# Kernel optimization log

Hardware: AMD Instinct MI355X
Metric: run time of the kernel (lower is better)

Reference implementation:

```python
import jax, jax.numpy as jnp
import numpy as np

N, K, D = 50000, 32, 128


def setup_inputs() -> dict:
    key = jax.random.key(0)
    k1, k2, k3, k4 = jax.random.split(key, 4)
    v_fea = jax.random.normal(k1, (N, D), dtype=jnp.float32)
    t_emb = jax.random.normal(k2, (N, D), dtype=jnp.float32)
    ef = jax.random.randint(k3, (N, K), 0, N, dtype=jnp.int64)
    # nn.Linear(2D, 2D, bias=False) weight, scaled like torch default init
    W = jax.random.normal(k4, (2 * D, 2 * D), dtype=jnp.float32) * (1.0 / np.sqrt(2 * D))
    return {"v_fea": v_fea, "t_emb": t_emb, "ef": ef, "W": W}


def reference(v_fea, t_emb, ef, W):
    # v: gathered neighbor features [N, K, D]
    v = v_fea[ef]
    # q: [N, 2D]; torch Linear applies x @ W.T
    q = jnp.concatenate([v_fea, t_emb], axis=-1)
    wq = q @ W.T                                   # [N, 2D]
    # k: [N, K, 2D]
    k = jnp.concatenate([v, t_emb[ef]], axis=-1)
    # per-edge score: bmm(k, wq[..., None]) -> [N, K]
    r = jnp.einsum("nkd,nd->nk", k, wq)
    r = jax.nn.softmax(r, axis=1)                  # softmax over neighbors
    # weighted sum over neighbors -> [N, D]
    ef_fea = jnp.einsum("nk,nkd->nd", r, v)
    return ef_fea
```

## Files before the change

kernel.cpp:

```cpp
#include <hip/hip_runtime.h>
#include <hip/hip_bf16.h>

#define D     128
#define TWO_D 256
#define KNB   32

typedef __attribute__((ext_vector_type(8))) short    s8;
typedef __attribute__((ext_vector_type(8))) _Float16 h8;
typedef __attribute__((ext_vector_type(2))) _Float16 h2v;
typedef __attribute__((ext_vector_type(4))) float    f4;

__device__ inline unsigned short f2h(float f) {
    return __builtin_bit_cast(unsigned short, (_Float16)f);
}
__device__ inline float h2f(unsigned short u) {
    return (float)__builtin_bit_cast(_Float16, u);
}

union v16u { s8 s; h2v h[4]; };

__device__ inline float dot8(s8 x, s8 w, float acc) {
#if __has_builtin(__builtin_amdgcn_fdot2)
    v16u ux, uw; ux.s = x; uw.s = w;
#pragma unroll
    for (int j = 0; j < 4; ++j)
        acc = __builtin_amdgcn_fdot2(ux.h[j], uw.h[j], acc, false);
#else
#pragma unroll
    for (int j = 0; j < 8; ++j)
        acc = fmaf(h2f((unsigned short)x[j]), h2f((unsigned short)w[j]), acc);
#endif
    return acc;
}

__global__ __launch_bounds__(256) void cast_kernel(
    const float* __restrict__ a, const float* __restrict__ b,
    unsigned short* __restrict__ oa, unsigned short* __restrict__ ob, int n4)
{
    int i = blockIdx.x * 256 + threadIdx.x;
    if (i >= n4) return;
    float4 x = ((const float4*)a)[i];
    float4 y = ((const float4*)b)[i];
    ushort4 px = make_ushort4(f2h(x.x), f2h(x.y), f2h(x.z), f2h(x.w));
    ushort4 py = make_ushort4(f2h(y.x), f2h(y.y), f2h(y.z), f2h(y.w));
    ((ushort4*)oa)[i] = px;
    ((ushort4*)ob)[i] = py;
}

#define BM 128
#define BN 128
#define BK 32
#define LDT 56

__global__ __launch_bounds__(256) void gemm_wq_mfma(
    const unsigned short* __restrict__ vh, const unsigned short* __restrict__ th,
    const float* __restrict__ W, unsigned short* __restrict__ wq_h, int M)
{
    __shared__ unsigned short As[BM][LDT];
    __shared__ unsigned short Bs[BN][LDT];

    const int tid  = threadIdx.x;
    const int w    = tid >> 6;
    const int lane = tid & 63;
    const int quad = lane >> 4;
    const int l16  = lane & 15;
    const int row0 = blockIdx.x * BM;
    const int i0   = blockIdx.y * BN;

    f4 acc[2][8] = {};

    const int srow = tid >> 1;
    const int seg  = tid & 1;
    int ga = row0 + srow; if (ga >= M) ga = M - 1;

    for (int kt = 0; kt < TWO_D; kt += BK) {
        const unsigned short* srcA = (kt < D) ? vh : th;
        const int kb = kt & (D - 1);
        const unsigned short* pa = srcA + (size_t)ga * D + kb + seg * 16;
        s8 a0 = *(const s8*)(pa);
        s8 a1 = *(const s8*)(pa + 8);
        const float* pb = W + (size_t)(i0 + srow) * TWO_D + kt + seg * 16;
        float4 b0 = *(const float4*)(pb);
        float4 b1 = *(const float4*)(pb + 4);
        float4 b2 = *(const float4*)(pb + 8);
        float4 b3 = *(const float4*)(pb + 12);

        __syncthreads();
        *(s8*)&As[srow][seg * 16]     = a0;
        *(s8*)&As[srow][seg * 16 + 8] = a1;
        {
            s8 q0, q1;
            q0[0]=(short)f2h(b0.x); q0[1]=(short)f2h(b0.y); q0[2]=(short)f2h(b0.z); q0[3]=(short)f2h(b0.w);
            q0[4]=(short)f2h(b1.x); q0[5]=(short)f2h(b1.y); q0[6]=(short)f2h(b1.z); q0[7]=(short)f2h(b1.w);
            q1[0]=(short)f2h(b2.x); q1[1]=(short)f2h(b2.y); q1[2]=(short)f2h(b2.z); q1[3]=(short)f2h(b2.w);
            q1[4]=(short)f2h(b3.x); q1[5]=(short)f2h(b3.y); q1[6]=(short)f2h(b3.z); q1[7]=(short)f2h(b3.w);
            *(s8*)&Bs[srow][seg * 16]     = q0;
            *(s8*)&Bs[srow][seg * 16 + 8] = q1;
        }
        __syncthreads();

        s8 af0 = *(const s8*)&As[w * 32 + l16][quad * 8];
        s8 af1 = *(const s8*)&As[w * 32 + 16 + l16][quad * 8];
#pragma unroll
        for (int nt = 0; nt < 8; ++nt) {
            s8 bf = *(const s8*)&Bs[nt * 16 + l16][quad * 8];
            acc[0][nt] = __builtin_amdgcn_mfma_f32_16x16x32_f16(
                __builtin_bit_cast(h8, af0), __builtin_bit_cast(h8, bf), acc[0][nt], 0, 0, 0);
            acc[1][nt] = __builtin_amdgcn_mfma_f32_16x16x32_f16(
                __builtin_bit_cast(h8, af1), __builtin_bit_cast(h8, bf), acc[1][nt], 0, 0, 0);
        }
    }

#pragma unroll
    for (int mt = 0; mt < 2; ++mt) {
#pragma unroll
        for (int nt = 0; nt < 8; ++nt) {
#pragma unroll
            for (int r = 0; r < 4; ++r) {
                int grow = row0 + w * 32 + mt * 16 + quad * 4 + r;
                if (grow < M)
                    wq_h[(size_t)grow * TWO_D + i0 + nt * 16 + l16] = f2h(acc[mt][nt][r]);
            }
        }
    }
}

__global__ __launch_bounds__(256) void attn_kernel(
    const unsigned short* __restrict__ vh, const unsigned short* __restrict__ th,
    const int* __restrict__ ef, const unsigned short* __restrict__ wq_h,
    float* __restrict__ outp, int M)
{
    __shared__ unsigned short v_cache[4][KNB][D];

    const int lane = threadIdx.x & 63;
    const int w    = threadIdx.x >> 6;
    const int n    = blockIdx.x * 4 + w;
    if (n >= M) return;

    const int l16  = lane & 15;
    const int gsel = (lane >> 4) & 1;
    const unsigned short* gsrc = (lane < 32) ? vh : th;

    s8 wq8 = *(const s8*)(wq_h + (size_t)n * TWO_D + ((lane >> 5) << 7) + l16 * 8);

    int eidx = 0;
    if (lane < KNB) eidx = ef[n * KNB + lane];

    s8 xs[16];
#pragma unroll
    for (int kk = 0; kk < 16; ++kk) {
        int e = __shfl(eidx, 2 * kk + gsel, 64);
        xs[kk] = *(const s8*)(gsrc + (size_t)e * D + l16 * 8);
    }

    float myscore = -1e30f;
#pragma unroll
    for (int kk = 0; kk < 16; ++kk) {
        const int k = 2 * kk;
        if (lane < 32) *(s8*)&v_cache[w][k + gsel][l16 * 8] = xs[kk];
        float p = dot8(xs[kk], wq8, 0.f);
#pragma unroll
        for (int off = 8; off > 0; off >>= 1) p += __shfl_xor(p, off, 64);
        p += __shfl_xor(p, 32, 64);
        float po = __shfl_xor(p, 16, 64);
        float s_even = gsel ? po : p;
        float s_odd  = gsel ? p  : po;
        if (lane == k)     myscore = s_even;
        if (lane == k + 1) myscore = s_odd;
    }

    float mx = myscore;
#pragma unroll
    for (int off = 16; off > 0; off >>= 1) mx = fmaxf(mx, __shfl_xor(mx, off, 64));
    float ex  = __expf(myscore - mx);
    float sum = ex;
#pragma unroll
    for (int off = 16; off > 0; off >>= 1) sum += __shfl_xor(sum, off, 64);
    float r = ex / sum;

    float2 o = make_float2(0.f, 0.f);
#pragma unroll
    for (int k = 0; k < KNB; ++k) {
        float rk = __shfl(r, k, 64);
        unsigned int pq = *(const unsigned int*)&v_cache[w][k][lane * 2];
        o.x = fmaf(rk, h2f((unsigned short)(pq & 0xFFFFu)), o.x);
        o.y = fmaf(rk, h2f((unsigned short)(pq >> 16)), o.y);
    }
    *(float2*)(outp + (size_t)n * D + lane * 2) = o;
}

extern "C" void kernel_launch(void* const* d_in, const int* in_sizes, int n_in,
                              void* d_out, int out_size, void* d_ws, size_t ws_size,
                              hipStream_t stream)
{
    const float* v_fea = (const float*)d_in[0];
    const float* t_emb = (const float*)d_in[1];
    const int*   ef    = (const int*)d_in[2];
    const float* W     = (const float*)d_in[3];
    float* outp = (float*)d_out;

    const int M = in_sizes[0] / D;
    char* ws = (char*)d_ws;
    unsigned short* wq_h = (unsigned short*)ws;
    unsigned short* vh   = (unsigned short*)(ws + (size_t)M * TWO_D * 2);
    unsigned short* th   = (unsigned short*)(ws + (size_t)M * TWO_D * 2 + (size_t)M * D * 2);

    const int n4 = M * D / 4;
    cast_kernel<<<(n4 + 255) / 256, 256, 0, stream>>>(v_fea, t_emb, vh, th, n4);

    dim3 gg((M + BM - 1) / BM, TWO_D / BN);
    gemm_wq_mfma<<<gg, 256, 0, stream>>>(vh, th, W, wq_h, M);
    attn_kernel<<<(M + 3) / 4, 256, 0, stream>>>(vh, th, ef, wq_h, outp, M);
}
```

Baseline: 232.0 us.

## Gather neighbor rows directly into LDS and retile wq GEMM

The attention kernel now gathers the neighbor v and t rows and the wq row straight into shared memory with global_load_lds instead of staging them through registers. Each lane then computes one neighbor's full score with a rotated LDS read order, which replaces the per-neighbor shuffle reductions. The weighted sum is split across two half-waves and combined with one xor shuffle. The GEMM tile moves to BN=64 and BK=64, and blocks shrink to 128 threads holding two nodes each. The grid M/2 assumes M is even, and the __syncthreads sits after an early return, which is a risk if a block's waves diverge.

Result: slower. 238.6 us (+2.8%).

```diff
diff --git a/kernel.cpp b/kernel.cpp
--- a/kernel.cpp
+++ b/kernel.cpp
@@ -13,8 +13,8 @@
 __device__ inline unsigned short f2h(float f) {
     return __builtin_bit_cast(unsigned short, (_Float16)f);
 }
-__device__ inline float h2f(unsigned short u) {
-    return (float)__builtin_bit_cast(_Float16, u);
+__device__ inline float h2f(unsigned int u) {
+    return (float)__builtin_bit_cast(_Float16, (unsigned short)u);
 }
 
 union v16u { s8 s; h2v h[4]; };
@@ -31,6 +31,12 @@
         acc = fmaf(h2f((unsigned short)x[j]), h2f((unsigned short)w[j]), acc);
 #endif
     return acc;
+}
+
+__device__ __forceinline__ void gload16(const void* g, void* l) {
+    __builtin_amdgcn_global_load_lds(
+        (__attribute__((address_space(1))) void*)g,
+        (__attribute__((address_space(3))) void*)l, 16, 0, 0);
 }
 
 __global__ __launch_bounds__(256) void cast_kernel(
@@ -48,9 +54,9 @@
 }
 
 #define BM 128
-#define BN 128
-#define BK 32
-#define LDT 56
+#define BN 64
+#define BK 64
+#define LDT 72
 
 __global__ __launch_bounds__(256) void gemm_wq_mfma(
     const unsigned short* __restrict__ vh, const unsigned short* __restrict__ th,
@@ -67,54 +73,63 @@
     const int row0 = blockIdx.x * BM;
     const int i0   = blockIdx.y * BN;
 
-    f4 acc[2][8] = {};
-
-    const int srow = tid >> 1;
-    const int seg  = tid & 1;
-    int ga = row0 + srow; if (ga >= M) ga = M - 1;
+    f4 acc[2][4] = {};
+
+    const int arow = tid >> 1;
+    const int acol = (tid & 1) * 32;
+    int ga = row0 + arow; if (ga >= M) ga = M - 1;
+    const int brow = tid >> 2;
+    const int bcol = (tid & 3) * 16;
 
     for (int kt = 0; kt < TWO_D; kt += BK) {
         const unsigned short* srcA = (kt < D) ? vh : th;
         const int kb = kt & (D - 1);
-        const unsigned short* pa = srcA + (size_t)ga * D + kb + seg * 16;
+        const unsigned short* pa = srcA + (size_t)ga * D + kb + acol;
         s8 a0 = *(const s8*)(pa);
         s8 a1 = *(const s8*)(pa + 8);
-        const float* pb = W + (size_t)(i0 + srow) * TWO_D + kt + seg * 16;
+        s8 a2 = *(const s8*)(pa + 16);
+        s8 a3 = *(const s8*)(pa + 24);
+        const float* pb = W + (size_t)(i0 + brow) * TWO_D + kt + bcol;
         float4 b0 = *(const float4*)(pb);
         float4 b1 = *(const float4*)(pb + 4);
         float4 b2 = *(const float4*)(pb + 8);
         float4 b3 = *(const float4*)(pb + 12);
 
         __syncthreads();
-        *(s8*)&As[srow][seg * 16]     = a0;
-        *(s8*)&As[srow][seg * 16 + 8] = a1;
+        *(s8*)&As[arow][acol]      = a0;
+        *(s8*)&As[arow][acol + 8]  = a1;
+        *(s8*)&As[arow][acol + 16] = a2;
+        *(s8*)&As[arow][acol + 24] = a3;
         {
             s8 q0, q1;
             q0[0]=(short)f2h(b0.x); q0[1]=(short)f2h(b0.y); q0[2]=(short)f2h(b0.z); q0[3]=(short)f2h(b0.w);
             q0[4]=(short)f2h(b1.x); q0[5]=(short)f2h(b1.y); q0[6]=(short)f2h(b1.z); q0[7]=(short)f2h(b1.w);
             q1[0]=(short)f2h(b2.x); q1[1]=(short)f2h(b2.y); q1[2]=(short)f2h(b2.z); q1[3]=(short)f2h(b2.w);
             q1[4]=(short)f2h(b3.x); q1[5]=(short)f2h(b3.y); q1[6]=(short)f2h(b3.z); q1[7]=(short)f2h(b3.w);
-            *(s8*)&Bs[srow][seg * 16]     = q0;
-            *(s8*)&Bs[srow][seg * 16 + 8] = q1;
+            *(s8*)&Bs[brow][bcol]     = q0;
+            *(s8*)&Bs[brow][bcol + 8] = q1;
         }
         __syncthreads();
 
-        s8 af0 = *(const s8*)&As[w * 32 + l16][quad * 8];
-        s8 af1 = *(const s8*)&As[w * 32 + 16 + l16][quad * 8];
-#pragma unroll
-        for (int nt = 0; nt < 8; ++nt) {
-            s8 bf = *(const s8*)&Bs[nt * 16 + l16][quad * 8];
-            acc[0][nt] = __builtin_amdgcn_mfma_f32_16x16x32_f16(
-                __builtin_bit_cast(h8, af0), __builtin_bit_cast(h8, bf), acc[0][nt], 0, 0, 0);
-            acc[1][nt] = __builtin_amdgcn_mfma_f32_16x16x32_f16(
-                __builtin_bit_cast(h8, af1), __builtin_bit_cast(h8, bf), acc[1][nt], 0, 0, 0);
+#pragma unroll
+        for (int s = 0; s < 2; ++s) {
+            s8 af0 = *(const s8*)&As[w * 32 + l16][s * 32 + quad * 8];
+            s8 af1 = *(const s8*)&As[w * 32 + 16 + l16][s * 32 + quad * 8];
+#pragma unroll
+            for (int nt = 0; nt < 4; ++nt) {
+                s8 bf = *(const s8*)&Bs[nt * 16 + l16][s * 32 + quad * 8];
+                acc[0][nt] = __builtin_amdgcn_mfma_f32_16x16x32_f16(
+                    __builtin_bit_cast(h8, af0), __builtin_bit_cast(h8, bf), acc[0][nt], 0, 0, 0);
+                acc[1][nt] = __builtin_amdgcn_mfma_f32_16x16x32_f16(
+                    __builtin_bit_cast(h8, af1), __builtin_bit_cast(h8, bf), acc[1][nt], 0, 0, 0);
+            }
         }
     }
 
 #pragma unroll
     for (int mt = 0; mt < 2; ++mt) {
 #pragma unroll
-        for (int nt = 0; nt < 8; ++nt) {
+        for (int nt = 0; nt < 4; ++nt) {
 #pragma unroll
             for (int r = 0; r < 4; ++r) {
                 int grow = row0 + w * 32 + mt * 16 + quad * 4 + r;
@@ -125,68 +140,75 @@
     }
 }
 
-__global__ __launch_bounds__(256) void attn_kernel(
+__global__ __launch_bounds__(128) void attn_kernel(
     const unsigned short* __restrict__ vh, const unsigned short* __restrict__ th,
     const int* __restrict__ ef, const unsigned short* __restrict__ wq_h,
     float* __restrict__ outp, int M)
 {
-    __shared__ unsigned short v_cache[4][KNB][D];
+    __shared__ char L[2][17408];
 
     const int lane = threadIdx.x & 63;
     const int w    = threadIdx.x >> 6;
-    const int n    = blockIdx.x * 4 + w;
+    const int n    = blockIdx.x * 2 + w;
     if (n >= M) return;
 
+    char* Lw = &L[w][0];
     const int l16  = lane & 15;
     const int gsel = (lane >> 4) & 1;
     const unsigned short* gsrc = (lane < 32) ? vh : th;
 
-    s8 wq8 = *(const s8*)(wq_h + (size_t)n * TWO_D + ((lane >> 5) << 7) + l16 * 8);
-
     int eidx = 0;
     if (lane < KNB) eidx = ef[n * KNB + lane];
 
-    s8 xs[16];
+    gload16(wq_h + (size_t)n * TWO_D + lane * 8, Lw + 16384);
 #pragma unroll
     for (int kk = 0; kk < 16; ++kk) {
         int e = __shfl(eidx, 2 * kk + gsel, 64);
-        xs[kk] = *(const s8*)(gsrc + (size_t)e * D + l16 * 8);
-    }
-
-    float myscore = -1e30f;
-#pragma unroll
-    for (int kk = 0; kk < 16; ++kk) {
-        const int k = 2 * kk;
-        if (lane < 32) *(s8*)&v_cache[w][k + gsel][l16 * 8] = xs[kk];
-        float p = dot8(xs[kk], wq8, 0.f);
-#pragma unroll
-        for (int off = 8; off > 0; off >>= 1) p += __shfl_xor(p, off, 64);
-        p += __shfl_xor(p, 32, 64);
-        float po = __shfl_xor(p, 16, 64);
-        float s_even = gsel ? po : p;
-        float s_odd  = gsel ? p  : po;
-        if (lane == k)     myscore = s_even;
-        if (lane == k + 1) myscore = s_odd;
-    }
-
-    float mx = myscore;
+        gload16(gsrc + (size_t)e * D + l16 * 8, Lw + kk * 1024);
+    }
+    __syncthreads();
+
+    const int k     = lane & 31;
+    const int tsel  = lane >> 5;
+    const int dbase = (k >> 1) * 1024 + (k & 1) * 256 + tsel * 512;
+    const int cbase = 16384 + tsel * 256;
+    float p = 0.f;
+#pragma unroll
+    for (int j = 0; j < 16; ++j) {
+        int jl = ((j + lane) & 15) * 16;
+        s8 x = *(const s8*)(Lw + dbase + jl);
+        s8 c = *(const s8*)(Lw + cbase + jl);
+        p = dot8(x, c, p);
+    }
+    p += __shfl_xor(p, 32, 64);
+
+    float mx = p;
 #pragma unroll
     for (int off = 16; off > 0; off >>= 1) mx = fmaxf(mx, __shfl_xor(mx, off, 64));
-    float ex  = __expf(myscore - mx);
+    float ex  = __expf(p - mx);
     float sum = ex;
 #pragma unroll
     for (int off = 16; off > 0; off >>= 1) sum += __shfl_xor(sum, off, 64);
     float r = ex / sum;
 
-    float2 o = make_float2(0.f, 0.f);
-#pragma unroll
-    for (int k = 0; k < KNB; ++k) {
-        float rk = __shfl(r, k, 64);
-        unsigned int pq = *(const unsigned int*)&v_cache[w][k][lane * 2];
-        o.x = fmaf(rk, h2f((unsigned short)(pq & 0xFFFFu)), o.x);
-        o.y = fmaf(rk, h2f((unsigned short)(pq >> 16)), o.y);
-    }
-    *(float2*)(outp + (size_t)n * D + lane * 2) = o;
+    float o4[4] = {0.f, 0.f, 0.f, 0.f};
+    const int g   = lane >> 5;
+    const int dby = (lane & 31) * 8;
+#pragma unroll
+    for (int kk = 0; kk < 16; ++kk) {
+        float rk = __shfl(r, 2 * kk + g, 64);
+        uint2 pq = *(const uint2*)(Lw + kk * 1024 + g * 256 + dby);
+        o4[0] = fmaf(rk, h2f(pq.x & 0xFFFFu), o4[0]);
+        o4[1] = fmaf(rk, h2f(pq.x >> 16),     o4[1]);
+        o4[2] = fmaf(rk, h2f(pq.y & 0xFFFFu), o4[2]);
+        o4[3] = fmaf(rk, h2f(pq.y >> 16),     o4[3]);
+    }
+#pragma unroll
+    for (int j = 0; j < 4; ++j) o4[j] += __shfl_xor(o4[j], 32, 64);
+
+    if (lane < 32)
+        *(float4*)(outp + (size_t)n * D + (lane & 31) * 4) =
+            make_float4(o4[0], o4[1], o4[2], o4[3]);
 }
 
 extern "C" void kernel_launch(void* const* d_in, const int* in_sizes, int n_in,
@@ -210,5 +232,5 @@
 
     dim3 gg((M + BM - 1) / BM, TWO_D / BN);
     gemm_wq_mfma<<<gg, 256, 0, stream>>>(vh, th, W, wq_h, M);
-    attn_kernel<<<(M + 3) / 4, 256, 0, stream>>>(vh, th, ef, wq_h, outp, M);
-}
+    attn_kernel<<<M / 2, 128, 0, stream>>>(vh, th, ef, wq_h, outp, M);
+}
```
